# Performance work log

Hardware: AMD Instinct MI355X
Metric: run time of the kernel (lower is better)

The kernel has to match this reference:

```python
import jax, jax.numpy as jnp
import numpy as np

B, N, D = 8, 256, 16   # batch, set size, in_dim
HID = 256              # hidden width (hidden_dims[:-1])
H = 128                # attention feature dim (hidden_dims[-1])
DH = 64                # per-dim feature dim d_h
NH = 4                 # attention heads


def _made_masks():
    in_deg = np.arange(1, D + 1)
    h_deg = (np.arange(HID) % (D - 1)) + 1
    out_deg = np.repeat(in_deg, H)  # per-dim contiguous layout -> reshape(..., D, H)
    m0 = h_deg[None, :] >= in_deg[:, None]
    m1 = h_deg[None, :] >= h_deg[:, None]
    m2 = out_deg[None, :] > h_deg[:, None]
    return jnp.array(m0), jnp.array(m1), jnp.array(m2)


def setup_inputs() -> dict:
    key = jax.random.key(0)
    ks = iter(jax.random.split(key, 40))
    def w(fi, fo):
        return jax.random.normal(next(ks), (fi, fo), jnp.float32) / np.sqrt(fi)
    inp = {"t": jnp.array([0.5], jnp.float32),
           "x": jax.random.normal(next(ks), (B, N, D), jnp.float32)}
    qd = [D, HID, HID, H * D]
    kd = [D, HID, HID, H]
    dd = [DH + 2, HID, HID, H, 1]
    for i in range(3):
        inp[f"q_w{i}"] = w(qd[i], qd[i + 1]); inp[f"q_b{i}"] = jnp.zeros((qd[i + 1],), jnp.float32)
        inp[f"k_w{i}"] = w(kd[i], kd[i + 1]); inp[f"k_b{i}"] = jnp.zeros((kd[i + 1],), jnp.float32)
        inp[f"v_w{i}"] = w(kd[i], kd[i + 1]); inp[f"v_b{i}"] = jnp.zeros((kd[i + 1],), jnp.float32)
    inp["p_w"] = w(H, DH); inp["p_b"] = jnp.zeros((DH,), jnp.float32)
    for i in range(4):
        inp[f"d_w{i}"] = w(dd[i], dd[i + 1]); inp[f"d_b{i}"] = jnp.zeros((dd[i + 1],), jnp.float32)
    inp["q_m0"], inp["q_m1"], inp["q_m2"] = _made_masks()
    return inp


def reference(t, x, q_w0, q_b0, k_w0, k_b0, v_w0, v_b0, q_w1, q_b1, k_w1, k_b1, v_w1, v_b1,
              q_w2, q_b2, k_w2, k_b2, v_w2, v_b2, p_w, p_b,
              d_w0, d_b0, d_w1, d_b1, d_w2, d_b2, d_w3, d_b3, q_m0, q_m1, q_m2):
    # --- exclusive net: MADE query (hollow per dim), MLP key/value, diagonal-masked attention ---
    hq = jax.nn.relu(x @ (q_w0 * q_m0) + q_b0)
    hq = jax.nn.relu(hq @ (q_w1 * q_m1) + q_b1)
    q = (hq @ (q_w2 * q_m2) + q_b2).reshape(B, N, D, H)      # [B,N,D,H]

    def mlp3(z, w0, b0, w1, b1, w2, b2):
        z = jnp.tanh(z @ w0 + b0)
        z = jnp.tanh(z @ w1 + b1)
        return z @ w2 + b2

    k = mlp3(x, k_w0, k_b0, k_w1, k_b1, k_w2, k_b2)          # [B,N,H] (shared across dims)
    v = mlp3(x, v_w0, v_b0, v_w1, v_b1, v_w2, v_b2)          # [B,N,H]

    dh = H // NH
    qh = q.transpose(0, 2, 1, 3).reshape(B, D, N, NH, dh).transpose(0, 1, 3, 2, 4)  # [B,D,NH,N,dh]
    kh = k.reshape(B, N, NH, dh).transpose(0, 2, 1, 3)        # [B,NH,N,dh]
    vh = v.reshape(B, N, NH, dh).transpose(0, 2, 1, 3)

    # einsum avoids materializing the repeat_interleaved key/value (same math)
    scores = jnp.einsum('bdhnc,bhmc->bdhnm', qh, kh) / np.sqrt(dh)
    scores = jnp.where(jnp.eye(N, dtype=bool), -jnp.inf, scores)  # mask self-attention (hollow)
    att = jax.nn.softmax(scores, axis=-1)
    o = jnp.einsum('bdhnm,bhmc->bdhnc', att, vh)              # [B,D,NH,N,dh]
    o = o.transpose(0, 1, 3, 2, 4).reshape(B, D, N, H).transpose(0, 2, 1, 3)  # [B,N,D,H]
    hfeat = o @ p_w + p_b                                     # [B,N,D,DH], hollow wrt x[...,d]

    # --- dimwise net: y_d = MLP([t, x_d, h_d]); exact diagonal Jacobian via jvp on x channel ---
    tb = jnp.broadcast_to(t.reshape(()), (B, N, D, 1)).astype(x.dtype)
    def dimwise(xc):
        z = jnp.concatenate([tb, xc, hfeat], -1)              # [B,N,D,2+DH]
        z = jnp.tanh(z @ d_w0 + d_b0)
        z = jnp.tanh(z @ d_w1 + d_b1)
        z = jnp.tanh(z @ d_w2 + d_b2)
        return (z @ d_w3 + d_b3)[..., 0]                      # [B,N,D]

    y, jac = jax.jvp(dimwise, (x[..., None],), (jnp.ones((B, N, D, 1), x.dtype),))
    return y, jac
```

## Files before the change

### kernel.cpp

```cpp
#include <hip/hip_runtime.h>
#include <hip/hip_bf16.h>

constexpr int kB = 8, kN = 256, kD = 16, kHID = 256, kH = 128, kDH = 64, kdh = 32;
constexpr int kBN = kB * kN;
constexpr int kP  = kBN * kD;

__device__ __forceinline__ float b2f(__hip_bfloat16 v) { return __bfloat162float(v); }
__device__ __forceinline__ __hip_bfloat16 f2b(float v) { return __float2bfloat16(v); }
__device__ __forceinline__ unsigned short f2bs(float v) {
    __hip_bfloat16 h = __float2bfloat16(v);
    return *(unsigned short*)&h;
}

__device__ __forceinline__ float tanh_fast(float v) {
    float e = __expf(2.f * v);
    return 1.f - 2.f * __builtin_amdgcn_rcpf(e + 1.f);
}

typedef short s8v  __attribute__((ext_vector_type(8)));
typedef float f4v  __attribute__((ext_vector_type(4)));
#define MFMA(a, b, c) __builtin_amdgcn_mfma_f32_16x16x32_bf16((a), (b), (c), 0, 0, 0)

__global__ __launch_bounds__(256) void prep_frag(
    const float* p_w, const float* d_w0, const float* d_w1, const float* d_w2,
    const float* k_w0, const float* k_w1, const float* k_w2,
    const float* v_w0, const float* v_w1, const float* v_w2,
    const float* q_w0, const float* q_w1, const float* q_w2,
    __hip_bfloat16* pwf, __hip_bfloat16* w0f, __hip_bfloat16* w1f, __hip_bfloat16* w2f,
    __hip_bfloat16* k0f, __hip_bfloat16* k1f, __hip_bfloat16* k2f,
    __hip_bfloat16* v0f, __hip_bfloat16* v1f, __hip_bfloat16* v2f,
    __hip_bfloat16* q0f, __hip_bfloat16* q1f, __hip_bfloat16* q2f)
{
    const int tile = blockIdx.x * 4 + (threadIdx.x >> 6);
    const int lane = threadIdx.x & 63;
    const float* src; __hip_bfloat16* dst; int N, NT, local, Kreal = 1 << 30, mask = 0;
    if (tile < 16)        { src = p_w;        dst = pwf; N = 64;   NT = 4;   local = tile; }
    else if (tile < 48)   { src = d_w0 + 512; dst = w0f; N = 256;  NT = 16;  local = tile - 16; }
    else if (tile < 176)  { src = d_w1;       dst = w1f; N = 256;  NT = 16;  local = tile - 48; }
    else if (tile < 240)  { src = d_w2;       dst = w2f; N = 128;  NT = 8;   local = tile - 176; }
    else if (tile < 256)  { src = k_w0;       dst = k0f; N = 256;  NT = 16;  local = tile - 240; Kreal = 16; }
    else if (tile < 272)  { src = v_w0;       dst = v0f; N = 256;  NT = 16;  local = tile - 256; Kreal = 16; }
    else if (tile < 288)  { src = q_w0;       dst = q0f; N = 256;  NT = 16;  local = tile - 272; Kreal = 16; mask = 1; }
    else if (tile < 416)  { src = k_w1;       dst = k1f; N = 256;  NT = 16;  local = tile - 288; }
    else if (tile < 544)  { src = v_w1;       dst = v1f; N = 256;  NT = 16;  local = tile - 416; }
    else if (tile < 672)  { src = q_w1;       dst = q1f; N = 256;  NT = 16;  local = tile - 544; mask = 2; }
    else if (tile < 736)  { src = k_w2;       dst = k2f; N = 128;  NT = 8;   local = tile - 672; }
    else if (tile < 800)  { src = v_w2;       dst = v2f; N = 128;  NT = 8;   local = tile - 736; }
    else                  { src = q_w2;       dst = q2f; N = 2048; NT = 128; local = tile - 800; mask = 3; }
    const int kt = local / NT, nt = local % NT;
    const int row0 = kt * 32 + (lane >> 4) * 8;
    const int col  = nt * 16 + (lane & 15);
    __hip_bfloat16* o = dst + ((size_t)local * 64 + lane) * 8;
    #pragma unroll
    for (int j = 0; j < 8; ++j) {
        const int r = row0 + j;
        float w = (r < Kreal) ? src[(size_t)r * N + col] : 0.f;
        if (mask == 1 && !((col % 15) >= r))        w = 0.f;
        if (mask == 2 && !((col % 15) >= (r % 15))) w = 0.f;
        if (mask == 3 && !((col >> 7) > (r % 15)))  w = 0.f;
        o[j] = f2b(w);
    }
}

__global__ __launch_bounds__(256) void mlp_kernel(
    const float* x,
    const float* k_b0, const float* k_b1, const float* k_b2,
    const float* v_b0, const float* v_b1, const float* v_b2,
    const float* q_b0, const float* q_b1,
    const __hip_bfloat16* k0f, const __hip_bfloat16* k1f, const __hip_bfloat16* k2f,
    const __hip_bfloat16* v0f, const __hip_bfloat16* v1f, const __hip_bfloat16* v2f,
    const __hip_bfloat16* q0f, const __hip_bfloat16* q1f,
    __hip_bfloat16* kbufF, __hip_bfloat16* vbufF, __hip_bfloat16* h1qF)
{
    constexpr int SA = 264;
    constexpr int SX = 40;
    __shared__ __hip_bfloat16 xin[32 * SX];
    __shared__ __hip_bfloat16 bufA[32 * SA];
    __shared__ __hip_bfloat16 bufB[32 * SA];

    const int tid  = threadIdx.x;
    const int wv   = tid >> 6, lane = tid & 63;
    const int lx   = lane & 15, quad = lane >> 4;
    const int path = blockIdx.x >> 6;
    const int r0   = (blockIdx.x & 63) * 32;

    auto ldA = [&](const __hip_bfloat16* buf, int stride, int m0, int k0) -> s8v {
        return *(const s8v*)(buf + (m0 + lx) * stride + k0 + quad * 8);
    };
    auto ldB = [&](const __hip_bfloat16* wf, int NT, int kt, int nt) -> s8v {
        return *(const s8v*)(wf + (((size_t)(kt * NT + nt) * 64 + lane) << 3));
    };

    for (int idx = tid; idx < 1024; idx += 256) {
        const int row = idx >> 5, c = idx & 31;
        xin[row * SX + c] = f2b(c < 16 ? x[(r0 + row) * kD + c] : 0.f);
    }

    const __hip_bfloat16* F0[3] = { k0f, v0f, q0f };
    const __hip_bfloat16* F1[3] = { k1f, v1f, q1f };
    const __hip_bfloat16* F2[2] = { k2f, v2f };
    const float* Ba0[3] = { k_b0, v_b0, q_b0 };
    const float* Ba1[3] = { k_b1, v_b1, q_b1 };
    const float* Ba2[2] = { k_b2, v_b2 };

    __syncthreads();

    {
        f4v acc[4][2] = {};
        const s8v a0 = ldA(xin, SX, 0, 0);
        const s8v a1 = ldA(xin, SX, 16, 0);
        #pragma unroll
        for (int j = 0; j < 4; ++j) {
            s8v b = ldB(F0[path], 16, 0, wv * 4 + j);
            acc[j][0] = MFMA(a0, b, acc[j][0]);
            acc[j][1] = MFMA(a1, b, acc[j][1]);
        }
        #pragma unroll
        for (int j = 0; j < 4; ++j) {
            const int n = (wv * 4 + j) * 16 + lx;
            const float bb = Ba0[path][n];
            #pragma unroll
            for (int mt = 0; mt < 2; ++mt)
            #pragma unroll
            for (int r = 0; r < 4; ++r) {
                const float v = acc[j][mt][r] + bb;
                const float z = (path == 2) ? fmaxf(v, 0.f) : tanh_fast(v);
                bufA[(mt * 16 + quad * 4 + r) * SA + n] = f2b(z);
            }
        }
    }
    __syncthreads();

    {
        f4v acc[4][2] = {};
        #pragma unroll
        for (int kt = 0; kt < 8; ++kt) {
            const s8v a0 = ldA(bufA, SA, 0, kt * 32);
            const s8v a1 = ldA(bufA, SA, 16, kt * 32);
            #pragma unroll
            for (int j = 0; j < 4; ++j) {
                s8v b = ldB(F1[path], 16, kt, wv * 4 + j);
                acc[j][0] = MFMA(a0, b, acc[j][0]);
                acc[j][1] = MFMA(a1, b, acc[j][1]);
            }
        }
        #pragma unroll
        for (int j = 0; j < 4; ++j) {
            const int n = (wv * 4 + j) * 16 + lx;
            const float bb = Ba1[path][n];
            #pragma unroll
            for (int mt = 0; mt < 2; ++mt)
            #pragma unroll
            for (int r = 0; r < 4; ++r) {
                const int m = mt * 16 + quad * 4 + r;
                const float v = acc[j][mt][r] + bb;
                if (path == 2) {
                    const int kt2 = (wv * 4 + j) >> 1;
                    const int q2  = ((wv * 4 + j) & 1) * 2 + (lx >> 3);
                    h1qF[(size_t)(((r0 >> 4) + mt) * 8 + kt2) * 512
                         + (q2 * 16 + quad * 4 + r) * 8 + (lx & 7)] = f2b(fmaxf(v, 0.f));
                } else {
                    bufB[m * SA + n] = f2b(tanh_fast(v));
                }
            }
        }
    }
    if (path == 2) return;
    __syncthreads();

    {
        f4v acc[2][2] = {};
        #pragma unroll
        for (int kt = 0; kt < 8; ++kt) {
            const s8v a0 = ldA(bufB, SA, 0, kt * 32);
            const s8v a1 = ldA(bufB, SA, 16, kt * 32);
            #pragma unroll
            for (int j = 0; j < 2; ++j) {
                s8v b = ldB(F2[path], 8, kt, wv * 2 + j);
                acc[j][0] = MFMA(a0, b, acc[j][0]);
                acc[j][1] = MFMA(a1, b, acc[j][1]);
            }
        }
        const int bidx = r0 >> 8;
        const int ktv  = (r0 >> 5) & 7;
        #pragma unroll
        for (int j = 0; j < 2; ++j) {
            const int n  = (wv * 2 + j) * 16 + lx;
            const float bb = Ba2[path][n];
            const int hd = n >> 5;
            #pragma unroll
            for (int mt = 0; mt < 2; ++mt)
            #pragma unroll
            for (int r = 0; r < 4; ++r) {
                const int gr = r0 + mt * 16 + quad * 4 + r;
                const __hip_bfloat16 hv = f2b(acc[j][mt][r] + bb);
                if (path == 0) {
                    const int mtg = (gr >> 4) & 15;
                    kbufF[(size_t)(((bidx * 4 + hd) * 16 + mtg) * 64
                          + ((n & 31) >> 3) * 16 + (gr & 15)) * 8 + (lx & 7)] = hv;
                } else {
                    const int m5 = gr & 31;
                    vbufF[(size_t)((((bidx * 4 + hd) * 2 + ((n >> 4) & 1)) * 8 + ktv) * 64
                          + (m5 >> 3) * 16 + lx) * 8 + (m5 & 7)] = hv;
                }
            }
        }
    }
}

__global__ __launch_bounds__(256, 2) void attn_kernel(
    const float* q_b2, const __hip_bfloat16* h1qF, const __hip_bfloat16* q2f,
    const __hip_bfloat16* kbufF, const __hip_bfloat16* vbufF,
    __hip_bfloat16* obuf)
{
    constexpr int SP = 264;
    constexpr int QP = 40;
    __shared__ short Pl[4][16 * SP];
    __shared__ short Qw[256 * QP];

    const int blk = blockIdx.x;
    const int hd = blk & 3;
    const int d  = (blk >> 2) & 15;
    const int b  = blk >> 6;

    const int wv   = threadIdx.x >> 6;
    const int lane = threadIdx.x & 63;
    const int lx = lane & 15, quad = lane >> 4;
    short* Pw = &Pl[wv][0];

    const short* hq = (const short*)h1qF;
    const short* kb = (const short*)kbufF;
    const short* vb = (const short*)vbufF;
    const int bh = b * 4 + hd;

    f4v qacc[4][2] = {};
    #pragma unroll
    for (int kt = 0; kt < 8; ++kt) {
        const s8v b0 = *(const s8v*)(q2f + (((size_t)(kt * 128 + d * 8 + hd * 2 + 0) * 64 + lane) << 3));
        const s8v b1 = *(const s8v*)(q2f + (((size_t)(kt * 128 + d * 8 + hd * 2 + 1) * 64 + lane) << 3));
        #pragma unroll
        for (int mt = 0; mt < 4; ++mt) {
            const s8v a = *(const s8v*)(hq + ((size_t)((b * 16 + wv * 4 + mt) * 8 + kt) * 512 + lane * 8));
            qacc[mt][0] = MFMA(a, b0, qacc[mt][0]);
            qacc[mt][1] = MFMA(a, b1, qacc[mt][1]);
        }
    }

    s8v kfrag[16];
    #pragma unroll
    for (int mt = 0; mt < 16; ++mt)
        kfrag[mt] = *(const s8v*)(kb + ((size_t)(bh * 16 + mt) * 64 + lane) * 8);
    s8v vfrag[2][8];
    #pragma unroll
    for (int ntv = 0; ntv < 2; ++ntv)
    #pragma unroll
    for (int kt = 0; kt < 8; ++kt)
        vfrag[ntv][kt] = *(const s8v*)(vb + ((size_t)((bh * 2 + ntv) * 8 + kt) * 64 + lane) * 8);

    {
        const float scale = 0.17677669529663687f;
        #pragma unroll
        for (int jn = 0; jn < 2; ++jn) {
            const float bb = q_b2[d * 128 + hd * 32 + jn * 16 + lx];
            #pragma unroll
            for (int mt = 0; mt < 4; ++mt)
            #pragma unroll
            for (int r = 0; r < 4; ++r) {
                const int lrow = wv * 64 + mt * 16 + quad * 4 + r;
                Qw[lrow * QP + jn * 16 + lx] = (short)f2bs((qacc[mt][jn][r] + bb) * scale);
            }
        }
    }
    __syncthreads();

    const float LOG2E = 1.4426950408889634f;

    for (int mi = 0; mi < 4; ++mi) {
        const int q0 = wv * 64 + mi * 16;

        const s8v qfrag = *(const s8v*)(Qw + (q0 + lx) * QP + quad * 8);

        f4v acc[16];
        #pragma unroll
        for (int mt = 0; mt < 16; ++mt) acc[mt] = f4v{0.f, 0.f, 0.f, 0.f};
        #pragma unroll
        for (int mt = 0; mt < 16; ++mt) acc[mt] = MFMA(kfrag[mt], qfrag, acc[mt]);

        const int qg = q0 + lx;
        float mx = -3.0e38f;
        #pragma unroll
        for (int mt = 0; mt < 16; ++mt)
        #pragma unroll
        for (int r = 0; r < 4; ++r) {
            const int key = mt * 16 + quad * 4 + r;
            float s = (key == qg) ? -3.0e38f : acc[mt][r];
            acc[mt][r] = s;
            mx = fmaxf(mx, s);
        }
        mx = fmaxf(mx, __shfl_xor(mx, 16, 64));
        mx = fmaxf(mx, __shfl_xor(mx, 32, 64));

        const float nmxc = -mx * LOG2E;
        float l = 0.f;
        #pragma unroll
        for (int mt = 0; mt < 16; ++mt)
        #pragma unroll
        for (int r = 0; r < 4; ++r) {
            float p = exp2f(__builtin_fmaf(acc[mt][r], LOG2E, nmxc));
            acc[mt][r] = p;
            l += p;
        }
        l += __shfl_xor(l, 16, 64);
        l += __shfl_xor(l, 32, 64);

        #pragma unroll
        for (int mt = 0; mt < 16; ++mt) {
            unsigned short h0 = f2bs(acc[mt][0]);
            unsigned short h1 = f2bs(acc[mt][1]);
            unsigned short h2 = f2bs(acc[mt][2]);
            unsigned short h3 = f2bs(acc[mt][3]);
            uint2 w;
            w.x = (unsigned int)h0 | ((unsigned int)h1 << 16);
            w.y = (unsigned int)h2 | ((unsigned int)h3 << 16);
            *(uint2*)(Pw + lx * SP + mt * 16 + quad * 4) = w;
        }
        __asm__ volatile("s_waitcnt lgkmcnt(0)" ::: "memory");

        f4v av[2] = { f4v{0.f,0.f,0.f,0.f}, f4v{0.f,0.f,0.f,0.f} };
        #pragma unroll
        for (int kt = 0; kt < 8; ++kt) {
            s8v a = *(const s8v*)(Pw + lx * SP + kt * 32 + quad * 8);
            av[0] = MFMA(a, vfrag[0][kt], av[0]);
            av[1] = MFMA(a, vfrag[1][kt], av[1]);
        }
        __asm__ volatile("s_waitcnt lgkmcnt(0)" ::: "memory");

        #pragma unroll
        for (int r = 0; r < 4; ++r) {
            const float lr = __shfl(l, quad * 4 + r, 64);
            const float inv = __builtin_amdgcn_rcpf(lr);
            const int qrow = q0 + quad * 4 + r;
            #pragma unroll
            for (int ntv = 0; ntv < 2; ++ntv) {
                obuf[((size_t)((b * 256 + qrow) * 16 + d)) * 128 + hd * 32 + ntv * 16 + lx]
                    = f2b(av[ntv][r] * inv);
            }
        }
    }
}

__global__ __launch_bounds__(256) void dim_kernel(
    const float* t, const float* x,
    const float* p_b, const float* d_w0, const float* d_b0,
    const float* d_b1, const float* d_b2, const float* d_w3, const float* d_b3,
    const __hip_bfloat16* pwf, const __hip_bfloat16* w0f,
    const __hip_bfloat16* w1f, const __hip_bfloat16* w2f,
    const __hip_bfloat16* obuf, float* out)
{
    constexpr int SA = 264;
    constexpr int SO = 136;
    constexpr int SH = 72;
    __shared__ __hip_bfloat16 bufA[32 * SA];
    __shared__ __hip_bfloat16 bufB[32 * SA];
    __shared__ __hip_bfloat16 bufH[16 * SH];
    __shared__ float xvs[16];

    const int tid  = threadIdx.x;
    const int wv   = tid >> 6, lane = tid & 63;
    const int lx   = lane & 15, quad = lane >> 4;
    const int p0   = blockIdx.x * 16;
    const float tval = t[0];

    auto ldA = [&](const __hip_bfloat16* buf, int stride, int m0, int k0) -> s8v {
        return *(const s8v*)(buf + (m0 + lx) * stride + k0 + quad * 8);
    };
    auto ldBf = [&](const __hip_bfloat16* wf, int NT, int kt, int nt) -> s8v {
        return *(const s8v*)(wf + (((size_t)(kt * NT + nt) * 64 + lane) << 3));
    };

    for (int idx = tid; idx < 256; idx += 256) {
        const int row = idx >> 4, ch = idx & 15;
        *(f4v*)(bufA + row * SO + ch * 8) = *(const f4v*)(obuf + (size_t)(p0 + row) * kH + ch * 8);
    }
    if (tid < 16) xvs[tid] = x[p0 + tid];
    __syncthreads();

    {
        f4v acc0 = {};
        #pragma unroll
        for (int ktile = 0; ktile < 4; ++ktile) {
            s8v b  = ldBf(pwf, 4, ktile, wv);
            s8v a0 = ldA(bufA, SO, 0, ktile * 32);
            acc0 = MFMA(a0, b, acc0);
        }
        const int n = wv * 16 + lx;
        const float bb = p_b[n];
        #pragma unroll
        for (int r = 0; r < 4; ++r)
            bufH[(quad * 4 + r) * SH + n] = f2b(acc0[r] + bb);
    }
    __syncthreads();

    {
        f4v acc[4] = {};
        #pragma unroll
        for (int ktile = 0; ktile < 2; ++ktile) {
            s8v a0 = ldA(bufH, SH, 0, ktile * 32);
            #pragma unroll
            for (int j = 0; j < 4; ++j) {
                s8v b = ldBf(w0f, 16, ktile, wv * 4 + j);
                acc[j] = MFMA(a0, b, acc[j]);
            }
        }
        #pragma unroll
        for (int j = 0; j < 4; ++j) {
            const int n = (wv * 4 + j) * 16 + lx;
            const float base = d_b0[n] + tval * d_w0[n];
            const float wx   = d_w0[256 + n];
            #pragma unroll
            for (int r = 0; r < 4; ++r) {
                const int m = quad * 4 + r;
                const float z = tanh_fast(acc[j][r] + base + xvs[m] * wx);
                bufB[m * SA + n]        = f2b(z);
                bufB[(m + 16) * SA + n] = f2b((1.f - z * z) * wx);
            }
        }
    }
    __syncthreads();

    {
        f4v acc[4][2] = {};
        #pragma unroll
        for (int ktile = 0; ktile < 8; ++ktile) {
            s8v a0 = ldA(bufB, SA, 0,  ktile * 32);
            s8v a1 = ldA(bufB, SA, 16, ktile * 32);
            #pragma unroll
            for (int j = 0; j < 4; ++j) {
                s8v b = ldBf(w1f, 16, ktile, wv * 4 + j);
                acc[j][0] = MFMA(a0, b, acc[j][0]);
                acc[j][1] = MFMA(a1, b, acc[j][1]);
            }
        }
        #pragma unroll
        for (int j = 0; j < 4; ++j) {
            const int n = (wv * 4 + j) * 16 + lx;
            const float b1 = d_b1[n];
            #pragma unroll
            for (int r = 0; r < 4; ++r) {
                const int m = quad * 4 + r;
                const float z  = tanh_fast(acc[j][0][r] + b1);
                const float zd = (1.f - z * z) * acc[j][1][r];
                bufA[m * SA + n]        = f2b(z);
                bufA[(m + 16) * SA + n] = f2b(zd);
            }
        }
    }
    __syncthreads();

    {
        f4v acc[2][2] = {};
        #pragma unroll
        for (int ktile = 0; ktile < 8; ++ktile) {
            s8v a0 = ldA(bufA, SA, 0,  ktile * 32);
            s8v a1 = ldA(bufA, SA, 16, ktile * 32);
            #pragma unroll
            for (int j = 0; j < 2; ++j) {
                s8v b = ldBf(w2f, 8, ktile, wv * 2 + j);
                acc[j][0] = MFMA(a0, b, acc[j][0]);
                acc[j][1] = MFMA(a1, b, acc[j][1]);
            }
        }
        #pragma unroll
        for (int j = 0; j < 2; ++j) {
            const int n = (wv * 2 + j) * 16 + lx;
            const float b2 = d_b2[n];
            #pragma unroll
            for (int r = 0; r < 4; ++r) {
                const int m = quad * 4 + r;
                const float z  = tanh_fast(acc[j][0][r] + b2);
                const float zd = (1.f - z * z) * acc[j][1][r];
                bufB[m * SO + n]        = f2b(z);
                bufB[(m + 16) * SO + n] = f2b(zd);
            }
        }
    }
    __syncthreads();

    {
        const int p = tid >> 4, s = tid & 15;
        float yv = 0.f, jv = 0.f;
        #pragma unroll
        for (int i = 0; i < 8; ++i) {
            const int n = s + i * 16;
            const float w = d_w3[n];
            yv += b2f(bufB[p * SO + n]) * w;
            jv += b2f(bufB[(p + 16) * SO + n]) * w;
        }
        #pragma unroll
        for (int off = 8; off > 0; off >>= 1) {
            yv += __shfl_down(yv, off, 16);
            jv += __shfl_down(jv, off, 16);
        }
        if (s == 0) {
            out[p0 + p]      = yv + d_b3[0];
            out[kP + p0 + p] = jv;
        }
    }
}

extern "C" void kernel_launch(void* const* d_in, const int* in_sizes, int n_in,
                              void* d_out, int out_size, void* d_ws, size_t ws_size,
                              hipStream_t stream)
{
    typedef const float* fp;
    fp t    = (fp)d_in[0];
    fp x    = (fp)d_in[1];
    fp q_w0 = (fp)d_in[2],  q_b0 = (fp)d_in[3];
    fp k_w0 = (fp)d_in[4],  k_b0 = (fp)d_in[5];
    fp v_w0 = (fp)d_in[6],  v_b0 = (fp)d_in[7];
    fp q_w1 = (fp)d_in[8],  q_b1 = (fp)d_in[9];
    fp k_w1 = (fp)d_in[10], k_b1 = (fp)d_in[11];
    fp v_w1 = (fp)d_in[12], v_b1 = (fp)d_in[13];
    fp q_w2 = (fp)d_in[14], q_b2 = (fp)d_in[15];
    fp k_w2 = (fp)d_in[16], k_b2 = (fp)d_in[17];
    fp v_w2 = (fp)d_in[18], v_b2 = (fp)d_in[19];
    fp p_w  = (fp)d_in[20], p_b  = (fp)d_in[21];
    fp d_w0 = (fp)d_in[22], d_b0 = (fp)d_in[23];
    fp d_w1 = (fp)d_in[24], d_b1 = (fp)d_in[25];
    fp d_w2 = (fp)d_in[26], d_b2 = (fp)d_in[27];
    fp d_w3 = (fp)d_in[28], d_b3 = (fp)d_in[29];

    __hip_bfloat16* wsb   = (__hip_bfloat16*)d_ws;
    __hip_bfloat16* kbufF = wsb;
    __hip_bfloat16* vbufF = kbufF + (size_t)kBN * kH;
    __hip_bfloat16* obuf  = vbufF + (size_t)kBN * kH;
    __hip_bfloat16* pwf   = obuf + (size_t)kP * kH;
    __hip_bfloat16* w0f   = pwf + 8192;
    __hip_bfloat16* w1f   = w0f + 16384;
    __hip_bfloat16* w2f   = w1f + 65536;
    __hip_bfloat16* k0f   = w2f + 32768;
    __hip_bfloat16* v0f   = k0f + 8192;
    __hip_bfloat16* q0f   = v0f + 8192;
    __hip_bfloat16* k1f   = q0f + 8192;
    __hip_bfloat16* v1f   = k1f + 65536;
    __hip_bfloat16* q1f   = v1f + 65536;
    __hip_bfloat16* k2f   = q1f + 65536;
    __hip_bfloat16* v2f   = k2f + 32768;
    __hip_bfloat16* q2f   = v2f + 32768;
    __hip_bfloat16* h1qF  = q2f + 524288;

    float* out = (float*)d_out;

    prep_frag<<<456, 256, 0, stream>>>(p_w, d_w0, d_w1, d_w2,
        k_w0, k_w1, k_w2, v_w0, v_w1, v_w2, q_w0, q_w1, q_w2,
        pwf, w0f, w1f, w2f, k0f, k1f, k2f, v0f, v1f, v2f, q0f, q1f, q2f);
    mlp_kernel<<<192, 256, 0, stream>>>(x,
        k_b0, k_b1, k_b2, v_b0, v_b1, v_b2, q_b0, q_b1,
        k0f, k1f, k2f, v0f, v1f, v2f, q0f, q1f, kbufF, vbufF, h1qF);
    attn_kernel<<<kB * kD * 4, 256, 0, stream>>>(q_b2, h1qF, q2f, kbufF, vbufF, obuf);
    dim_kernel<<<kP / 16, 256, 0, stream>>>(t, x, p_b, d_w0, d_b0, d_b1, d_b2, d_w3, d_b3,
        pwf, w0f, w1f, w2f, obuf, out);
}
```

Measured before the change: 189.4 us.

## Overlap weight-fragment prep with later kernels and double dim_kernel rows per block

Splits the monolithic weight-repacking kernel so that only the K/V/Q MLP weights are prepared first. The q_w2 fragments are packed by extra blocks appended to mlp_kernel, and the p_w/d_w fragments by extra blocks appended to attn_kernel, so that packing work runs in the same launch as useful compute. Kernel arguments are also consolidated into a single parameter struct. Separately, dim_kernel now processes 32 points per block instead of 16, reusing each loaded weight fragment across twice as many MFMA rows, at the cost of more shared memory and registers per block.

```diff
diff --git a/kernel.cpp b/kernel.cpp
--- a/kernel.cpp
+++ b/kernel.cpp
@@ -21,32 +21,34 @@
 typedef float f4v  __attribute__((ext_vector_type(4)));
 #define MFMA(a, b, c) __builtin_amdgcn_mfma_f32_16x16x32_bf16((a), (b), (c), 0, 0, 0)
 
-__global__ __launch_bounds__(256) void prep_frag(
-    const float* p_w, const float* d_w0, const float* d_w1, const float* d_w2,
-    const float* k_w0, const float* k_w1, const float* k_w2,
-    const float* v_w0, const float* v_w1, const float* v_w2,
-    const float* q_w0, const float* q_w1, const float* q_w2,
-    __hip_bfloat16* pwf, __hip_bfloat16* w0f, __hip_bfloat16* w1f, __hip_bfloat16* w2f,
-    __hip_bfloat16* k0f, __hip_bfloat16* k1f, __hip_bfloat16* k2f,
-    __hip_bfloat16* v0f, __hip_bfloat16* v1f, __hip_bfloat16* v2f,
-    __hip_bfloat16* q0f, __hip_bfloat16* q1f, __hip_bfloat16* q2f)
+struct KParams {
+    const float *t, *x;
+    const float *q_b0, *k_b0, *v_b0, *q_b1, *k_b1, *v_b1, *k_b2, *v_b2, *q_b2;
+    const float *p_w, *p_b;
+    const float *d_w0, *d_b0, *d_b1, *d_b2, *d_w3, *d_b3, *d_w1, *d_w2;
+    const float *k_w0, *k_w1, *k_w2, *v_w0, *v_w1, *v_w2, *q_w0, *q_w1, *q_w2;
+    __hip_bfloat16 *pwf, *w0f, *w1f, *w2f;
+    __hip_bfloat16 *k0f, *k1f, *k2f, *v0f, *v1f, *v2f, *q0f, *q1f, *q2f;
+    __hip_bfloat16 *kbufF, *vbufF, *h1qF, *obuf;
+    float *out;
+};
+
+__device__ __forceinline__ void prep_tile(const KParams& P, int tile, int lane)
 {
-    const int tile = blockIdx.x * 4 + (threadIdx.x >> 6);
-    const int lane = threadIdx.x & 63;
     const float* src; __hip_bfloat16* dst; int N, NT, local, Kreal = 1 << 30, mask = 0;
-    if (tile < 16)        { src = p_w;        dst = pwf; N = 64;   NT = 4;   local = tile; }
-    else if (tile < 48)   { src = d_w0 + 512; dst = w0f; N = 256;  NT = 16;  local = tile - 16; }
-    else if (tile < 176)  { src = d_w1;       dst = w1f; N = 256;  NT = 16;  local = tile - 48; }
-    else if (tile < 240)  { src = d_w2;       dst = w2f; N = 128;  NT = 8;   local = tile - 176; }
-    else if (tile < 256)  { src = k_w0;       dst = k0f; N = 256;  NT = 16;  local = tile - 240; Kreal = 16; }
-    else if (tile < 272)  { src = v_w0;       dst = v0f; N = 256;  NT = 16;  local = tile - 256; Kreal = 16; }
-    else if (tile < 288)  { src = q_w0;       dst = q0f; N = 256;  NT = 16;  local = tile - 272; Kreal = 16; mask = 1; }
-    else if (tile < 416)  { src = k_w1;       dst = k1f; N = 256;  NT = 16;  local = tile - 288; }
-    else if (tile < 544)  { src = v_w1;       dst = v1f; N = 256;  NT = 16;  local = tile - 416; }
-    else if (tile < 672)  { src = q_w1;       dst = q1f; N = 256;  NT = 16;  local = tile - 544; mask = 2; }
-    else if (tile < 736)  { src = k_w2;       dst = k2f; N = 128;  NT = 8;   local = tile - 672; }
-    else if (tile < 800)  { src = v_w2;       dst = v2f; N = 128;  NT = 8;   local = tile - 736; }
-    else                  { src = q_w2;       dst = q2f; N = 2048; NT = 128; local = tile - 800; mask = 3; }
+    if (tile < 16)        { src = P.p_w;        dst = P.pwf; N = 64;   NT = 4;   local = tile; }
+    else if (tile < 48)   { src = P.d_w0 + 512; dst = P.w0f; N = 256;  NT = 16;  local = tile - 16; }
+    else if (tile < 176)  { src = P.d_w1;       dst = P.w1f; N = 256;  NT = 16;  local = tile - 48; }
+    else if (tile < 240)  { src = P.d_w2;       dst = P.w2f; N = 128;  NT = 8;   local = tile - 176; }
+    else if (tile < 256)  { src = P.k_w0;       dst = P.k0f; N = 256;  NT = 16;  local = tile - 240; Kreal = 16; }
+    else if (tile < 272)  { src = P.v_w0;       dst = P.v0f; N = 256;  NT = 16;  local = tile - 256; Kreal = 16; }
+    else if (tile < 288)  { src = P.q_w0;       dst = P.q0f; N = 256;  NT = 16;  local = tile - 272; Kreal = 16; mask = 1; }
+    else if (tile < 416)  { src = P.k_w1;       dst = P.k1f; N = 256;  NT = 16;  local = tile - 288; }
+    else if (tile < 544)  { src = P.v_w1;       dst = P.v1f; N = 256;  NT = 16;  local = tile - 416; }
+    else if (tile < 672)  { src = P.q_w1;       dst = P.q1f; N = 256;  NT = 16;  local = tile - 544; mask = 2; }
+    else if (tile < 736)  { src = P.k_w2;       dst = P.k2f; N = 128;  NT = 8;   local = tile - 672; }
+    else if (tile < 800)  { src = P.v_w2;       dst = P.v2f; N = 128;  NT = 8;   local = tile - 736; }
+    else                  { src = P.q_w2;       dst = P.q2f; N = 2048; NT = 128; local = tile - 800; mask = 3; }
     const int kt = local / NT, nt = local % NT;
     const int row0 = kt * 32 + (lane >> 4) * 8;
     const int col  = nt * 16 + (lane & 15);
@@ -62,15 +64,13 @@
     }
 }
 
-__global__ __launch_bounds__(256) void mlp_kernel(
-    const float* x,
-    const float* k_b0, const float* k_b1, const float* k_b2,
-    const float* v_b0, const float* v_b1, const float* v_b2,
-    const float* q_b0, const float* q_b1,
-    const __hip_bfloat16* k0f, const __hip_bfloat16* k1f, const __hip_bfloat16* k2f,
-    const __hip_bfloat16* v0f, const __hip_bfloat16* v1f, const __hip_bfloat16* v2f,
-    const __hip_bfloat16* q0f, const __hip_bfloat16* q1f,
-    __hip_bfloat16* kbufF, __hip_bfloat16* vbufF, __hip_bfloat16* h1qF)
+__global__ __launch_bounds__(256) void prep_mlpw_kernel(KParams P)
+{
+    const int s = blockIdx.x * 4 + (threadIdx.x >> 6);
+    prep_tile(P, 240 + s, threadIdx.x & 63);
+}
+
+__global__ __launch_bounds__(256) void mlp_kernel(KParams P)
 {
     constexpr int SA = 264;
     constexpr int SX = 40;
@@ -80,6 +80,13 @@
 
     const int tid  = threadIdx.x;
     const int wv   = tid >> 6, lane = tid & 63;
+
+    if (blockIdx.x >= 192) {
+        const int s = (blockIdx.x - 192) * 4 + wv;
+        prep_tile(P, 800 + s, lane);
+        return;
+    }
+
     const int lx   = lane & 15, quad = lane >> 4;
     const int path = blockIdx.x >> 6;
     const int r0   = (blockIdx.x & 63) * 32;
@@ -93,15 +100,15 @@
 
     for (int idx = tid; idx < 1024; idx += 256) {
         const int row = idx >> 5, c = idx & 31;
-        xin[row * SX + c] = f2b(c < 16 ? x[(r0 + row) * kD + c] : 0.f);
-    }
-
-    const __hip_bfloat16* F0[3] = { k0f, v0f, q0f };
-    const __hip_bfloat16* F1[3] = { k1f, v1f, q1f };
-    const __hip_bfloat16* F2[2] = { k2f, v2f };
-    const float* Ba0[3] = { k_b0, v_b0, q_b0 };
-    const float* Ba1[3] = { k_b1, v_b1, q_b1 };
-    const float* Ba2[2] = { k_b2, v_b2 };
+        xin[row * SX + c] = f2b(c < 16 ? P.x[(r0 + row) * kD + c] : 0.f);
+    }
+
+    const __hip_bfloat16* F0[3] = { P.k0f, P.v0f, P.q0f };
+    const __hip_bfloat16* F1[3] = { P.k1f, P.v1f, P.q1f };
+    const __hip_bfloat16* F2[2] = { P.k2f, P.v2f };
+    const float* Ba0[3] = { P.k_b0, P.v_b0, P.q_b0 };
+    const float* Ba1[3] = { P.k_b1, P.v_b1, P.q_b1 };
+    const float* Ba2[2] = { P.k_b2, P.v_b2 };
 
     __syncthreads();
 
@@ -157,7 +164,7 @@
                 if (path == 2) {
                     const int kt2 = (wv * 4 + j) >> 1;
                     const int q2  = ((wv * 4 + j) & 1) * 2 + (lx >> 3);
-                    h1qF[(size_t)(((r0 >> 4) + mt) * 8 + kt2) * 512
+                    P.h1qF[(size_t)(((r0 >> 4) + mt) * 8 + kt2) * 512
                          + (q2 * 16 + quad * 4 + r) * 8 + (lx & 7)] = f2b(fmaxf(v, 0.f));
                 } else {
                     bufB[m * SA + n] = f2b(tanh_fast(v));
@@ -196,11 +203,11 @@
                 const __hip_bfloat16 hv = f2b(acc[j][mt][r] + bb);
                 if (path == 0) {
                     const int mtg = (gr >> 4) & 15;
-                    kbufF[(size_t)(((bidx * 4 + hd) * 16 + mtg) * 64
+                    P.kbufF[(size_t)(((bidx * 4 + hd) * 16 + mtg) * 64
                           + ((n & 31) >> 3) * 16 + (gr & 15)) * 8 + (lx & 7)] = hv;
                 } else {
                     const int m5 = gr & 31;
-                    vbufF[(size_t)((((bidx * 4 + hd) * 2 + ((n >> 4) & 1)) * 8 + ktv) * 64
+                    P.vbufF[(size_t)((((bidx * 4 + hd) * 2 + ((n >> 4) & 1)) * 8 + ktv) * 64
                           + (m5 >> 3) * 16 + lx) * 8 + (m5 & 7)] = hv;
                 }
             }
@@ -208,36 +215,40 @@
     }
 }
 
-__global__ __launch_bounds__(256, 2) void attn_kernel(
-    const float* q_b2, const __hip_bfloat16* h1qF, const __hip_bfloat16* q2f,
-    const __hip_bfloat16* kbufF, const __hip_bfloat16* vbufF,
-    __hip_bfloat16* obuf)
+__global__ __launch_bounds__(256, 2) void attn_kernel(KParams P)
 {
     constexpr int SP = 264;
     constexpr int QP = 40;
     __shared__ short Pl[4][16 * SP];
     __shared__ short Qw[256 * QP];
 
+    const int wv   = threadIdx.x >> 6;
+    const int lane = threadIdx.x & 63;
+
+    if (blockIdx.x >= 512) {
+        const int s = (blockIdx.x - 512) * 4 + wv;
+        prep_tile(P, s, lane);
+        return;
+    }
+
     const int blk = blockIdx.x;
     const int hd = blk & 3;
     const int d  = (blk >> 2) & 15;
     const int b  = blk >> 6;
 
-    const int wv   = threadIdx.x >> 6;
-    const int lane = threadIdx.x & 63;
     const int lx = lane & 15, quad = lane >> 4;
     short* Pw = &Pl[wv][0];
 
-    const short* hq = (const short*)h1qF;
-    const short* kb = (const short*)kbufF;
-    const short* vb = (const short*)vbufF;
+    const short* hq = (const short*)P.h1qF;
+    const short* kb = (const short*)P.kbufF;
+    const short* vb = (const short*)P.vbufF;
     const int bh = b * 4 + hd;
 
     f4v qacc[4][2] = {};
     #pragma unroll
     for (int kt = 0; kt < 8; ++kt) {
-        const s8v b0 = *(const s8v*)(q2f + (((size_t)(kt * 128 + d * 8 + hd * 2 + 0) * 64 + lane) << 3));
-        const s8v b1 = *(const s8v*)(q2f + (((size_t)(kt * 128 + d * 8 + hd * 2 + 1) * 64 + lane) << 3));
+        const s8v b0 = *(const s8v*)(P.q2f + (((size_t)(kt * 128 + d * 8 + hd * 2 + 0) * 64 + lane) << 3));
+        const s8v b1 = *(const s8v*)(P.q2f + (((size_t)(kt * 128 + d * 8 + hd * 2 + 1) * 64 + lane) << 3));
         #pragma unroll
         for (int mt = 0; mt < 4; ++mt) {
             const s8v a = *(const s8v*)(hq + ((size_t)((b * 16 + wv * 4 + mt) * 8 + kt) * 512 + lane * 8));
@@ -261,7 +272,7 @@
         const float scale = 0.17677669529663687f;
         #pragma unroll
         for (int jn = 0; jn < 2; ++jn) {
-            const float bb = q_b2[d * 128 + hd * 32 + jn * 16 + lx];
+            const float bb = P.q_b2[d * 128 + hd * 32 + jn * 16 + lx];
             #pragma unroll
             for (int mt = 0; mt < 4; ++mt)
             #pragma unroll
@@ -342,34 +353,28 @@
             const int qrow = q0 + quad * 4 + r;
             #pragma unroll
             for (int ntv = 0; ntv < 2; ++ntv) {
-                obuf[((size_t)((b * 256 + qrow) * 16 + d)) * 128 + hd * 32 + ntv * 16 + lx]
+                P.obuf[((size_t)((b * 256 + qrow) * 16 + d)) * 128 + hd * 32 + ntv * 16 + lx]
                     = f2b(av[ntv][r] * inv);
             }
         }
     }
 }
 
-__global__ __launch_bounds__(256) void dim_kernel(
-    const float* t, const float* x,
-    const float* p_b, const float* d_w0, const float* d_b0,
-    const float* d_b1, const float* d_b2, const float* d_w3, const float* d_b3,
-    const __hip_bfloat16* pwf, const __hip_bfloat16* w0f,
-    const __hip_bfloat16* w1f, const __hip_bfloat16* w2f,
-    const __hip_bfloat16* obuf, float* out)
+__global__ __launch_bounds__(256, 2) void dim_kernel(KParams P)
 {
     constexpr int SA = 264;
     constexpr int SO = 136;
     constexpr int SH = 72;
-    __shared__ __hip_bfloat16 bufA[32 * SA];
-    __shared__ __hip_bfloat16 bufB[32 * SA];
-    __shared__ __hip_bfloat16 bufH[16 * SH];
-    __shared__ float xvs[16];
+    __shared__ __hip_bfloat16 bufA[64 * SA];
+    __shared__ __hip_bfloat16 bufB[64 * SA];
+    __shared__ __hip_bfloat16 bufH[32 * SH];
+    __shared__ float xvs[32];
 
     const int tid  = threadIdx.x;
     const int wv   = tid >> 6, lane = tid & 63;
     const int lx   = lane & 15, quad = lane >> 4;
-    const int p0   = blockIdx.x * 16;
-    const float tval = t[0];
+    const int p0   = blockIdx.x * 32;
+    const float tval = P.t[0];
 
     auto ldA = [&](const __hip_bfloat16* buf, int stride, int m0, int k0) -> s8v {
         return *(const s8v*)(buf + (m0 + lx) * stride + k0 + quad * 8);
@@ -378,132 +383,152 @@
         return *(const s8v*)(wf + (((size_t)(kt * NT + nt) * 64 + lane) << 3));
     };
 
-    for (int idx = tid; idx < 256; idx += 256) {
+    for (int idx = tid; idx < 512; idx += 256) {
         const int row = idx >> 4, ch = idx & 15;
-        *(f4v*)(bufA + row * SO + ch * 8) = *(const f4v*)(obuf + (size_t)(p0 + row) * kH + ch * 8);
-    }
-    if (tid < 16) xvs[tid] = x[p0 + tid];
-    __syncthreads();
-
-    {
-        f4v acc0 = {};
+        *(f4v*)(bufA + row * SO + ch * 8) = *(const f4v*)(P.obuf + (size_t)(p0 + row) * kH + ch * 8);
+    }
+    if (tid < 32) xvs[tid] = P.x[p0 + tid];
+    __syncthreads();
+
+    {
+        f4v acc0 = {}, acc1 = {};
         #pragma unroll
         for (int ktile = 0; ktile < 4; ++ktile) {
-            s8v b  = ldBf(pwf, 4, ktile, wv);
-            s8v a0 = ldA(bufA, SO, 0, ktile * 32);
+            s8v b  = ldBf(P.pwf, 4, ktile, wv);
+            s8v a0 = ldA(bufA, SO, 0,  ktile * 32);
+            s8v a1 = ldA(bufA, SO, 16, ktile * 32);
             acc0 = MFMA(a0, b, acc0);
+            acc1 = MFMA(a1, b, acc1);
         }
         const int n = wv * 16 + lx;
-        const float bb = p_b[n];
-        #pragma unroll
-        for (int r = 0; r < 4; ++r)
-            bufH[(quad * 4 + r) * SH + n] = f2b(acc0[r] + bb);
-    }
-    __syncthreads();
-
-    {
-        f4v acc[4] = {};
+        const float bb = P.p_b[n];
+        #pragma unroll
+        for (int r = 0; r < 4; ++r) {
+            bufH[(quad * 4 + r) * SH + n]        = f2b(acc0[r] + bb);
+            bufH[(quad * 4 + r + 16) * SH + n]   = f2b(acc1[r] + bb);
+        }
+    }
+    __syncthreads();
+
+    {
+        f4v acc[4][2] = {};
         #pragma unroll
         for (int ktile = 0; ktile < 2; ++ktile) {
-            s8v a0 = ldA(bufH, SH, 0, ktile * 32);
+            s8v a0 = ldA(bufH, SH, 0,  ktile * 32);
+            s8v a1 = ldA(bufH, SH, 16, ktile * 32);
             #pragma unroll
             for (int j = 0; j < 4; ++j) {
-                s8v b = ldBf(w0f, 16, ktile, wv * 4 + j);
-                acc[j] = MFMA(a0, b, acc[j]);
+                s8v b = ldBf(P.w0f, 16, ktile, wv * 4 + j);
+                acc[j][0] = MFMA(a0, b, acc[j][0]);
+                acc[j][1] = MFMA(a1, b, acc[j][1]);
             }
         }
         #pragma unroll
         for (int j = 0; j < 4; ++j) {
             const int n = (wv * 4 + j) * 16 + lx;
-            const float base = d_b0[n] + tval * d_w0[n];
-            const float wx   = d_w0[256 + n];
-            #pragma unroll
-            for (int r = 0; r < 4; ++r) {
-                const int m = quad * 4 + r;
-                const float z = tanh_fast(acc[j][r] + base + xvs[m] * wx);
+            const float base = P.d_b0[n] + tval * P.d_w0[n];
+            const float wx   = P.d_w0[256 + n];
+            #pragma unroll
+            for (int mt = 0; mt < 2; ++mt)
+            #pragma unroll
+            for (int r = 0; r < 4; ++r) {
+                const int m = mt * 16 + quad * 4 + r;
+                const float z = tanh_fast(acc[j][mt][r] + base + xvs[m] * wx);
                 bufB[m * SA + n]        = f2b(z);
-                bufB[(m + 16) * SA + n] = f2b((1.f - z * z) * wx);
-            }
-        }
-    }
-    __syncthreads();
-
-    {
-        f4v acc[4][2] = {};
+                bufB[(m + 32) * SA + n] = f2b((1.f - z * z) * wx);
+            }
+        }
+    }
+    __syncthreads();
+
+    {
+        f4v acc[4][4] = {};
         #pragma unroll
         for (int ktile = 0; ktile < 8; ++ktile) {
             s8v a0 = ldA(bufB, SA, 0,  ktile * 32);
             s8v a1 = ldA(bufB, SA, 16, ktile * 32);
+            s8v a2 = ldA(bufB, SA, 32, ktile * 32);
+            s8v a3 = ldA(bufB, SA, 48, ktile * 32);
             #pragma unroll
             for (int j = 0; j < 4; ++j) {
-                s8v b = ldBf(w1f, 16, ktile, wv * 4 + j);
+                s8v b = ldBf(P.w1f, 16, ktile, wv * 4 + j);
                 acc[j][0] = MFMA(a0, b, acc[j][0]);
                 acc[j][1] = MFMA(a1, b, acc[j][1]);
+                acc[j][2] = MFMA(a2, b, acc[j][2]);
+                acc[j][3] = MFMA(a3, b, acc[j][3]);
             }
         }
         #pragma unroll
         for (int j = 0; j < 4; ++j) {
             const int n = (wv * 4 + j) * 16 + lx;
-            const float b1 = d_b1[n];
-            #pragma unroll
-            for (int r = 0; r < 4; ++r) {
-                const int m = quad * 4 + r;
-                const float z  = tanh_fast(acc[j][0][r] + b1);
-                const float zd = (1.f - z * z) * acc[j][1][r];
+            const float b1 = P.d_b1[n];
+            #pragma unroll
+            for (int mt = 0; mt < 2; ++mt)
+            #pragma unroll
+            for (int r = 0; r < 4; ++r) {
+                const int m = mt * 16 + quad * 4 + r;
+                const float z  = tanh_fast(acc[j][mt][r] + b1);
+                const float zd = (1.f - z * z) * acc[j][mt + 2][r];
                 bufA[m * SA + n]        = f2b(z);
-                bufA[(m + 16) * SA + n] = f2b(zd);
-            }
-        }
-    }
-    __syncthreads();
-
-    {
-        f4v acc[2][2] = {};
+                bufA[(m + 32) * SA + n] = f2b(zd);
+            }
+        }
+    }
+    __syncthreads();
+
+    {
+        f4v acc[2][4] = {};
         #pragma unroll
         for (int ktile = 0; ktile < 8; ++ktile) {
             s8v a0 = ldA(bufA, SA, 0,  ktile * 32);
             s8v a1 = ldA(bufA, SA, 16, ktile * 32);
+            s8v a2 = ldA(bufA, SA, 32, ktile * 32);
+            s8v a3 = ldA(bufA, SA, 48, ktile * 32);
             #pragma unroll
             for (int j = 0; j < 2; ++j) {
-                s8v b = ldBf(w2f, 8, ktile, wv * 2 + j);
+                s8v b = ldBf(P.w2f, 8, ktile, wv * 2 + j);
                 acc[j][0] = MFMA(a0, b, acc[j][0]);
                 acc[j][1] = MFMA(a1, b, acc[j][1]);
+                acc[j][2] = MFMA(a2, b, acc[j][2]);
+                acc[j][3] = MFMA(a3, b, acc[j][3]);
             }
         }
         #pragma unroll
         for (int j = 0; j < 2; ++j) {
             const int n = (wv * 2 + j) * 16 + lx;
-            const float b2 = d_b2[n];
-            #pragma unroll
-            for (int r = 0; r < 4; ++r) {
-                const int m = quad * 4 + r;
-                const float z  = tanh_fast(acc[j][0][r] + b2);
-                const float zd = (1.f - z * z) * acc[j][1][r];
+            const float b2 = P.d_b2[n];
+            #pragma unroll
+            for (int mt = 0; mt < 2; ++mt)
+            #pragma unroll
+            for (int r = 0; r < 4; ++r) {
+                const int m = mt * 16 + quad * 4 + r;
+                const float z  = tanh_fast(acc[j][mt][r] + b2);
+                const float zd = (1.f - z * z) * acc[j][mt + 2][r];
                 bufB[m * SO + n]        = f2b(z);
-                bufB[(m + 16) * SO + n] = f2b(zd);
-            }
-        }
-    }
-    __syncthreads();
-
-    {
-        const int p = tid >> 4, s = tid & 15;
+                bufB[(m + 32) * SO + n] = f2b(zd);
+            }
+        }
+    }
+    __syncthreads();
+
+    {
+        const int p = tid >> 3, s = tid & 7;
         float yv = 0.f, jv = 0.f;
         #pragma unroll
-        for (int i = 0; i < 8; ++i) {
-            const int n = s + i * 16;
-            const float w = d_w3[n];
+        for (int i = 0; i < 16; ++i) {
+            const int n = s + i * 8;
+            const float w = P.d_w3[n];
             yv += b2f(bufB[p * SO + n]) * w;
-            jv += b2f(bufB[(p + 16) * SO + n]) * w;
-        }
-        #pragma unroll
-        for (int off = 8; off > 0; off >>= 1) {
-            yv += __shfl_down(yv, off, 16);
-            jv += __shfl_down(jv, off, 16);
+            jv += b2f(bufB[(p + 32) * SO + n]) * w;
+        }
+        #pragma unroll
+        for (int off = 4; off > 0; off >>= 1) {
+            yv += __shfl_down(yv, off, 8);
+            jv += __shfl_down(jv, off, 8);
         }
         if (s == 0) {
-            out[p0 + p]      = yv + d_b3[0];
-            out[kP + p0 + p] = jv;
+            P.out[p0 + p]      = yv + P.d_b3[0];
+            P.out[kP + p0 + p] = jv;
         }
     }
 }
@@ -513,51 +538,46 @@
                               hipStream_t stream)
 {
     typedef const float* fp;
-    fp t    = (fp)d_in[0];
-    fp x    = (fp)d_in[1];
-    fp q_w0 = (fp)d_in[2],  q_b0 = (fp)d_in[3];
-    fp k_w0 = (fp)d_in[4],  k_b0 = (fp)d_in[5];
-    fp v_w0 = (fp)d_in[6],  v_b0 = (fp)d_in[7];
-    fp q_w1 = (fp)d_in[8],  q_b1 = (fp)d_in[9];
-    fp k_w1 = (fp)d_in[10], k_b1 = (fp)d_in[11];
-    fp v_w1 = (fp)d_in[12], v_b1 = (fp)d_in[13];
-    fp q_w2 = (fp)d_in[14], q_b2 = (fp)d_in[15];
-    fp k_w2 = (fp)d_in[16], k_b2 = (fp)d_in[17];
-    fp v_w2 = (fp)d_in[18], v_b2 = (fp)d_in[19];
-    fp p_w  = (fp)d_in[20], p_b  = (fp)d_in[21];
-    fp d_w0 = (fp)d_in[22], d_b0 = (fp)d_in[23];
-    fp d_w1 = (fp)d_in[24], d_b1 = (fp)d_in[25];
-    fp d_w2 = (fp)d_in[26], d_b2 = (fp)d_in[27];
-    fp d_w3 = (fp)d_in[28], d_b3 = (fp)d_in[29];
-
-    __hip_bfloat16* wsb   = (__hip_bfloat16*)d_ws;
-    __hip_bfloat16* kbufF = wsb;
-    __hip_bfloat16* vbufF = kbufF + (size_t)kBN * kH;
-    __hip_bfloat16* obuf  = vbufF + (size_t)kBN * kH;
-    __hip_bfloat16* pwf   = obuf + (size_t)kP * kH;
-    __hip_bfloat16* w0f   = pwf + 8192;
-    __hip_bfloat16* w1f   = w0f + 16384;
-    __hip_bfloat16* w2f   = w1f + 65536;
-    __hip_bfloat16* k0f   = w2f + 32768;
-    __hip_bfloat16* v0f   = k0f + 8192;
-    __hip_bfloat16* q0f   = v0f + 8192;
-    __hip_bfloat16* k1f   = q0f + 8192;
-    __hip_bfloat16* v1f   = k1f + 65536;
-    __hip_bfloat16* q1f   = v1f + 65536;
-    __hip_bfloat16* k2f   = q1f + 65536;
-    __hip_bfloat16* v2f   = k2f + 32768;
-    __hip_bfloat16* q2f   = v2f + 32768;
-    __hip_bfloat16* h1qF  = q2f + 524288;
-
-    float* out = (float*)d_out;
-
-    prep_frag<<<456, 256, 0, stream>>>(p_w, d_w0, d_w1, d_w2,
-        k_w0, k_w1, k_w2, v_w0, v_w1, v_w2, q_w0, q_w1, q_w2,
-        pwf, w0f, w1f, w2f, k0f, k1f, k2f, v0f, v1f, v2f, q0f, q1f, q2f);
-    mlp_kernel<<<192, 256, 0, stream>>>(x,
-        k_b0, k_b1, k_b2, v_b0, v_b1, v_b2, q_b0, q_b1,
-        k0f, k1f, k2f, v0f, v1f, v2f, q0f, q1f, kbufF, vbufF, h1qF);
-    attn_kernel<<<kB * kD * 4, 256, 0, stream>>>(q_b2, h1qF, q2f, kbufF, vbufF, obuf);
-    dim_kernel<<<kP / 16, 256, 0, stream>>>(t, x, p_b, d_w0, d_b0, d_b1, d_b2, d_w3, d_b3,
-        pwf, w0f, w1f, w2f, obuf, out);
-}
+    KParams P;
+    P.t    = (fp)d_in[0];
+    P.x    = (fp)d_in[1];
+    P.q_w0 = (fp)d_in[2];  P.q_b0 = (fp)d_in[3];
+    P.k_w0 = (fp)d_in[4];  P.k_b0 = (fp)d_in[5];
+    P.v_w0 = (fp)d_in[6];  P.v_b0 = (fp)d_in[7];
+    P.q_w1 = (fp)d_in[8];  P.q_b1 = (fp)d_in[9];
+    P.k_w1 = (fp)d_in[10]; P.k_b1 = (fp)d_in[11];
+    P.v_w1 = (fp)d_in[12]; P.v_b1 = (fp)d_in[13];
+    P.q_w2 = (fp)d_in[14]; P.q_b2 = (fp)d_in[15];
+    P.k_w2 = (fp)d_in[16]; P.k_b2 = (fp)d_in[17];
+    P.v_w2 = (fp)d_in[18]; P.v_b2 = (fp)d_in[19];
+    P.p_w  = (fp)d_in[20]; P.p_b  = (fp)d_in[21];
+    P.d_w0 = (fp)d_in[22]; P.d_b0 = (fp)d_in[23];
+    P.d_w1 = (fp)d_in[24]; P.d_b1 = (fp)d_in[25];
+    P.d_w2 = (fp)d_in[26]; P.d_b2 = (fp)d_in[27];
+    P.d_w3 = (fp)d_in[28]; P.d_b3 = (fp)d_in[29];
+
+    __hip_bfloat16* wsb = (__hip_bfloat16*)d_ws;
+    P.kbufF = wsb;
+    P.vbufF = P.kbufF + (size_t)kBN * kH;
+    P.obuf  = P.vbufF + (size_t)kBN * kH;
+    P.pwf   = P.obuf + (size_t)kP * kH;
+    P.w0f   = P.pwf + 8192;
+    P.w1f   = P.w0f + 16384;
+    P.w2f   = P.w1f + 65536;
+    P.k0f   = P.w2f + 32768;
+    P.v0f   = P.k0f + 8192;
+    P.q0f   = P.v0f + 8192;
+    P.k1f   = P.q0f + 8192;
+    P.v1f   = P.k1f + 65536;
+    P.q1f   = P.v1f + 65536;
+    P.k2f   = P.q1f + 65536;
+    P.v2f   = P.k2f + 32768;
+    P.q2f   = P.v2f + 32768;
+    P.h1qF  = P.q2f + 524288;
+    P.out   = (float*)d_out;
+
+    prep_mlpw_kernel<<<140, 256, 0, stream>>>(P);
+    mlp_kernel<<<448, 256, 0, stream>>>(P);
+    attn_kernel<<<572, 256, 0, stream>>>(P);
+    dim_kernel<<<kP / 32, 256, 0, stream>>>(P);
+}
```

Measured after the change: 192.4 us. About the same (+1.6%).
